# Optimization experiments

Measured on AMD Instinct MI355X. Metric: run time of the kernel, lower is better.

## Reference

```python
import jax, jax.numpy as jnp
import numpy as np

H = 64   # LSTM hidden size
NL = 8   # LSTM layers
B, T = 2048, 64


def setup_inputs() -> dict:
    key = jax.random.key(0)
    ks = jax.random.split(key, 18)
    r = lambda i, shape, s=0.1: jax.random.normal(ks[i], shape, dtype=jnp.float32) * s
    return {
        "x": r(0, (B, T, 2), 1.0),
        "w1": r(1, (16, 2)), "b1": r(2, (16,)),
        "w2": r(3, (16, 16)), "b2": r(4, (16,)),
        "w_ih0": r(5, (4 * H, 16)), "w_hh0": r(6, (4 * H, H)),
        "b_ih0": r(7, (4 * H,)), "b_hh0": r(8, (4 * H,)),
        "w_ih": r(9, (NL - 1, 4 * H, H)), "w_hh": r(10, (NL - 1, 4 * H, H)),
        "b_ih": r(11, (NL - 1, 4 * H)), "b_hh": r(12, (NL - 1, 4 * H)),
        "wo1": r(13, (32, H)), "bo1": r(14, (32,)),
        "wo2": r(15, (4, 32)), "bo2": r(16, (4,)),
    }


def _lstm_layer(x, w_ih, w_hh, b):
    # x: [B, T, I]; torch gate order: i, f, g, o
    bsz = x.shape[0]
    xg = jnp.einsum('bti,gi->btg', x, w_ih) + b  # [B, T, 4H] precomputed input gates

    def step(carry, xg_t):
        h, c = carry
        gates = xg_t + h @ w_hh.T
        i, f, g, o = jnp.split(gates, 4, axis=-1)
        i = jax.nn.sigmoid(i); f = jax.nn.sigmoid(f)
        g = jnp.tanh(g); o = jax.nn.sigmoid(o)
        c = f * c + i * g
        h = o * jnp.tanh(c)
        return (h, c), h

    h0 = jnp.zeros((bsz, H), x.dtype)
    _, hs = jax.lax.scan(step, (h0, h0), jnp.swapaxes(xg, 0, 1))  # [T, B, H]
    return jnp.swapaxes(hs, 0, 1)


def reference(x, w1, b1, w2, b2, w_ih0, w_hh0, b_ih0, b_hh0,
              w_ih, w_hh, b_ih, b_hh, wo1, bo1, wo2, bo2):
    # action-input MLP: 2 -> 16 -> relu -> 16
    h = jax.nn.relu(x @ w1.T + b1) @ w2.T + b2
    # 8-layer LSTM, hidden 64
    h = _lstm_layer(h, w_ih0, w_hh0, b_ih0 + b_hh0)
    for l in range(NL - 1):
        h = _lstm_layer(h, w_ih[l], w_hh[l], b_ih[l] + b_hh[l])
    # output MLP: 64 -> 32 -> relu -> 4
    return jax.nn.relu(h @ wo1.T + bo1) @ wo2.T + bo2
```

## Files before the change

kernel.cpp:

```cpp
#include <hip/hip_runtime.h>


#define BATCH 2048
#define TT 64
#define HH 64
#define LDP 136

typedef short bf16x8 __attribute__((ext_vector_type(8)));
typedef float f32x4 __attribute__((ext_vector_type(4)));

__device__ __forceinline__ float sigmoid_fast(float x) {
    return __builtin_amdgcn_rcpf(1.f + __expf(-x));
}
__device__ __forceinline__ float tanh_fast(float x) {
    float e = __expf(-2.f * x);
    e = fminf(e, 1e30f);
    return (1.f - e) * __builtin_amdgcn_rcpf(1.f + e);
}
__device__ __forceinline__ void split2(float x, unsigned short& hi, unsigned short& lo) {
    const unsigned u = __float_as_uint(x);
    hi = (unsigned short)(u >> 16);
    const float r = x - __uint_as_float(u & 0xFFFF0000u);
    lo = (unsigned short)(__float_as_uint(r) >> 16);
}
__device__ __forceinline__ void wg_wait(int* c, int v) {
    while (__hip_atomic_load(c, __ATOMIC_ACQUIRE, __HIP_MEMORY_SCOPE_WORKGROUP) < v) {}
}
__device__ __forceinline__ void wg_bump(int* c, int lane) {
    if (lane == 0)
        __hip_atomic_fetch_add(c, 1, __ATOMIC_RELEASE, __HIP_MEMORY_SCOPE_WORKGROUP);
}

__global__ __launch_bounds__(256)
void mlp_in_kernel(const float* __restrict__ x,
                   const float* __restrict__ w1, const float* __restrict__ b1,
                   const float* __restrict__ w2, const float* __restrict__ b2,
                   float* __restrict__ out) {
    const int gid = blockIdx.x * 256 + threadIdx.x;
    const float x0 = x[gid * 2 + 0];
    const float x1 = x[gid * 2 + 1];
    float hid[16];
#pragma unroll
    for (int j = 0; j < 16; ++j) {
        float v = fmaf(x1, w1[j * 2 + 1], fmaf(x0, w1[j * 2 + 0], b1[j]));
        hid[j] = fmaxf(0.f, v);
    }
    float o[16];
#pragma unroll
    for (int oo = 0; oo < 16; ++oo) {
        float acc = b2[oo];
#pragma unroll
        for (int j = 0; j < 16; ++j) acc = fmaf(hid[j], w2[oo * 16 + j], acc);
        o[oo] = acc;
    }
    float4* op = (float4*)(out + gid * 16);
#pragma unroll
    for (int q = 0; q < 4; ++q) {
        float4 v;
        v.x = o[q * 4 + 0]; v.y = o[q * 4 + 1]; v.z = o[q * 4 + 2]; v.w = o[q * 4 + 3];
        op[q] = v;
    }
}

template <int IA, int IPADA>
__global__ __launch_bounds__(512, 2)
void lstm_pair(const float* __restrict__ xmlp,
               unsigned* __restrict__ P,
               float* __restrict__ houtf,
               const int last,
               const float* __restrict__ wihA, const float* __restrict__ whhA,
               const float* __restrict__ biA, const float* __restrict__ bhA,
               const float* __restrict__ wihB, const float* __restrict__ whhB,
               const float* __restrict__ biB, const float* __restrict__ bhB) {
    constexpr int KTA = (IPADA + 64) / 32;
    constexpr int KTX = IPADA / 32;
    constexpr int LDPA = IPADA + 8;
    __shared__ __align__(16) unsigned short pAh[2][16 * LDPA], pAl[2][16 * LDPA];
    __shared__ __align__(16) unsigned short pBh[2][16 * LDP], pBl[2][16 * LDP];
    __shared__ int cA, cB;

    const int tid = threadIdx.x;
    const int wv = tid >> 6, lane = tid & 63, l16 = lane & 15, quad = lane >> 4;
    const int grp = wv >> 2;
    const int wg = wv & 3;
    const int base = blockIdx.x * 8;
    const bool lo32 = (lane < 32);
    const int bpi = (lane & 31) << 2;

    if (tid == 0) { cA = 0; cB = 0; }
    for (int e = tid; e < 2 * 16 * LDPA; e += 512) { (&pAh[0][0])[e] = 0; (&pAl[0][0])[e] = 0; }
    for (int e = tid; e < 2 * 16 * LDP; e += 512)  { (&pBh[0][0])[e] = 0; (&pBl[0][0])[e] = 0; }

    const int I    = grp ? 64 : IA;
    const int IPAD = grp ? 64 : IPADA;
    const int KT   = grp ? 4  : KTA;
    const float* wih = grp ? wihB : wihA;
    const float* whh = grp ? whhB : whhA;
    const float* bi  = grp ? biB  : biA;
    const float* bh  = grp ? bhB  : bhA;

    const int jg = 16 * wg + l16;
    bf16x8 bhi[4][4], blo[4][4];
    float bsum[4];
#pragma unroll
    for (int gt = 0; gt < 4; ++gt) {
        const int n = gt * 64 + jg;
        bsum[gt] = bi[n] + bh[n];
#pragma unroll
        for (int kt = 0; kt < 4; ++kt) {
            bf16x8 vh = {0, 0, 0, 0, 0, 0, 0, 0};
            bf16x8 vl = {0, 0, 0, 0, 0, 0, 0, 0};
            if (kt < KT) {
#pragma unroll
                for (int j = 0; j < 8; ++j) {
                    const int k = kt * 32 + quad * 8 + j;
                    float w = 0.f;
                    if (k < I) w = wih[n * I + k];
                    else if (k >= IPAD) w = whh[n * 64 + (k - IPAD)];
                    unsigned short h_, l_;
                    split2(w, h_, l_);
                    vh[j] = (short)h_;
                    vl[j] = (short)l_;
                }
            }
            bhi[kt][gt] = vh;
            blo[kt][gt] = vl;
        }
    }

    float cs[2] = {0.f, 0.f};
    const int row0 = (quad & 1) * 4 + ((quad >> 1) << 1);

    float2 xr2 = {0.f, 0.f};
    uint2 xru = {0u, 0u};
    int sr = 0, sc = 0;
    bool stg = false;
    if (grp == 0) {
        if (IA == 16) {
            stg = (tid < 128);
            sr = tid >> 3; sc = (tid & 7) * 2;
            if (stg) {
                xr2 = *(const float2*)&xmlp[((size_t)(base + sr) * TT + 0) * 16 + sc];
                unsigned short h0, l0, h1, l1;
                split2(xr2.x, h0, l0); split2(xr2.y, h1, l1);
                *(unsigned*)&pAh[0][sr * LDPA + sc] = ((unsigned)h1 << 16) | h0;
                *(unsigned*)&pAl[0][sr * LDPA + sc] = ((unsigned)l1 << 16) | l0;
                xr2 = *(const float2*)&xmlp[((size_t)(base + sr) * TT + 1) * 16 + sc];
            }
        } else {
            stg = true;
            sr = tid >> 5; sc = (tid & 31) * 2;
            xru = *(const uint2*)&P[((size_t)(base + sr) * TT + 0) * 64 + sc];
            *(unsigned*)&pAh[0][sr * LDPA + sc] = (xru.y & 0xFFFF0000u) | (xru.x >> 16);
            *(unsigned*)&pAl[0][sr * LDPA + sc] = (xru.y << 16) | (xru.x & 0xFFFFu);
            xru = *(const uint2*)&P[((size_t)(base + sr) * TT + 1) * 64 + sc];
        }
    }
    __syncthreads();

    if (grp == 0) {
        for (int t = 0; t < TT; ++t) {
            const int pb = t & 1;
            if (t) {
                wg_wait(&cA, 4 * t);
                if (t >= 2) wg_wait(&cB, 4 * (t - 1));
            }
            if (stg) {
                if (IA == 16) {
                    unsigned short h0, l0, h1, l1;
                    split2(xr2.x, h0, l0); split2(xr2.y, h1, l1);
                    *(unsigned*)&pAh[pb ^ 1][sr * LDPA + sc] = ((unsigned)h1 << 16) | h0;
                    *(unsigned*)&pAl[pb ^ 1][sr * LDPA + sc] = ((unsigned)l1 << 16) | l0;
                    const int tp = (t + 2) & (TT - 1);
                    xr2 = *(const float2*)&xmlp[((size_t)(base + sr) * TT + tp) * 16 + sc];
                } else {
                    *(unsigned*)&pAh[pb ^ 1][sr * LDPA + sc] = (xru.y & 0xFFFF0000u) | (xru.x >> 16);
                    *(unsigned*)&pAl[pb ^ 1][sr * LDPA + sc] = (xru.y << 16) | (xru.x & 0xFFFFu);
                    const int tp = (t + 2) & (TT - 1);
                    xru = *(const uint2*)&P[((size_t)(base + sr) * TT + tp) * 64 + sc];
                }
            }
            f32x4 a0[4], a1[4], a2[4];
#pragma unroll
            for (int gt = 0; gt < 4; ++gt) {
                a0[gt][0] = bsum[gt]; a0[gt][1] = bsum[gt];
                a0[gt][2] = bsum[gt]; a0[gt][3] = bsum[gt];
                a1[gt] = (f32x4){0.f, 0.f, 0.f, 0.f};
                a2[gt] = (f32x4){0.f, 0.f, 0.f, 0.f};
            }
            __builtin_amdgcn_s_setprio(1);
#pragma unroll
            for (int kt = 0; kt < KTA; ++kt) {
                bf16x8 ahi, alo;
                if (kt < KTX) {
                    const int aoff = l16 * LDPA + kt * 32 + quad * 8;
                    ahi = *(const bf16x8*)&pAh[pb][aoff];
                    alo = *(const bf16x8*)&pAl[pb][aoff];
                } else {
                    const int aoff = l16 * LDP + (kt - KTX) * 32 + quad * 8;
                    ahi = *(const bf16x8*)&pBh[pb ^ 1][aoff];
                    alo = *(const bf16x8*)&pBl[pb ^ 1][aoff];
                }
#pragma unroll
                for (int gt = 0; gt < 4; ++gt) {
                    a0[gt] = __builtin_amdgcn_mfma_f32_16x16x32_bf16(ahi, bhi[kt][gt], a0[gt], 0, 0, 0);
                    a1[gt] = __builtin_amdgcn_mfma_f32_16x16x32_bf16(alo, bhi[kt][gt], a1[gt], 0, 0, 0);
                    a2[gt] = __builtin_amdgcn_mfma_f32_16x16x32_bf16(ahi, blo[kt][gt], a2[gt], 0, 0, 0);
                }
            }
            __builtin_amdgcn_s_setprio(0);
            f32x4 s4[4];
#pragma unroll
            for (int gt = 0; gt < 4; ++gt) s4[gt] = (a0[gt] + a1[gt]) + a2[gt];
            float gk[4][2];
#pragma unroll
            for (int gt = 0; gt < 4; ++gt) {
#pragma unroll
                for (int r = 0; r < 2; ++r) {
                    const float up = __uint_as_float(
                        __builtin_amdgcn_ds_bpermute(bpi, __float_as_uint(s4[gt][r + 2])));
                    gk[gt][r] = lo32 ? s4[gt][r] : up;
                }
            }
#pragma unroll
            for (int r = 0; r < 2; ++r) {
                const float iv = sigmoid_fast(gk[0][r]);
                const float fv = sigmoid_fast(gk[1][r]);
                const float gv = tanh_fast(gk[2][r]);
                const float ov = sigmoid_fast(gk[3][r]);
                const float cn = fv * cs[r] + iv * gv;
                cs[r] = cn;
                const float h = ov * tanh_fast(cn);
                const int R = row0 + r;
                unsigned short h_, l_;
                split2(h, h_, l_);
                pBh[pb][R * LDP + jg] = h_;
                pBl[pb][R * LDP + jg] = l_;
            }
            wg_bump(&cA, lane);
        }
    } else {
        for (int t = 0; t < TT; ++t) {
            const int pb = t & 1;
            wg_wait(&cA, 4 * (t + 1));
            if (t) wg_wait(&cB, 4 * t);
            f32x4 a0[4], a1[4], a2[4];
#pragma unroll
            for (int gt = 0; gt < 4; ++gt) {
                a0[gt][0] = bsum[gt]; a0[gt][1] = bsum[gt];
                a0[gt][2] = bsum[gt]; a0[gt][3] = bsum[gt];
                a1[gt] = (f32x4){0.f, 0.f, 0.f, 0.f};
                a2[gt] = (f32x4){0.f, 0.f, 0.f, 0.f};
            }
            __builtin_amdgcn_s_setprio(1);
#pragma unroll
            for (int kt = 0; kt < 4; ++kt) {
                const int aoff = l16 * LDP + kt * 32 + quad * 8;
                const bf16x8 ahi = *(const bf16x8*)&pBh[pb][aoff];
                const bf16x8 alo = *(const bf16x8*)&pBl[pb][aoff];
#pragma unroll
                for (int gt = 0; gt < 4; ++gt) {
                    a0[gt] = __builtin_amdgcn_mfma_f32_16x16x32_bf16(ahi, bhi[kt][gt], a0[gt], 0, 0, 0);
                    a1[gt] = __builtin_amdgcn_mfma_f32_16x16x32_bf16(alo, bhi[kt][gt], a1[gt], 0, 0, 0);
                    a2[gt] = __builtin_amdgcn_mfma_f32_16x16x32_bf16(ahi, blo[kt][gt], a2[gt], 0, 0, 0);
                }
            }
            __builtin_amdgcn_s_setprio(0);
            f32x4 s4[4];
#pragma unroll
            for (int gt = 0; gt < 4; ++gt) s4[gt] = (a0[gt] + a1[gt]) + a2[gt];
            float gk[4][2];
#pragma unroll
            for (int gt = 0; gt < 4; ++gt) {
#pragma unroll
                for (int r = 0; r < 2; ++r) {
                    const float up = __uint_as_float(
                        __builtin_amdgcn_ds_bpermute(bpi, __float_as_uint(s4[gt][r + 2])));
                    gk[gt][r] = lo32 ? s4[gt][r] : up;
                }
            }
#pragma unroll
            for (int r = 0; r < 2; ++r) {
                const float iv = sigmoid_fast(gk[0][r]);
                const float fv = sigmoid_fast(gk[1][r]);
                const float gv = tanh_fast(gk[2][r]);
                const float ov = sigmoid_fast(gk[3][r]);
                const float cn = fv * cs[r] + iv * gv;
                cs[r] = cn;
                const float h = ov * tanh_fast(cn);
                const int R = row0 + r;
                unsigned short h_, l_;
                split2(h, h_, l_);
                pBh[pb ^ 1][R * LDP + 64 + jg] = h_;
                pBl[pb ^ 1][R * LDP + 64 + jg] = l_;
                if (!last) {
                    P[((size_t)(base + R) * TT + t) * 64 + jg] =
                        ((unsigned)h_ << 16) | (unsigned)l_;
                } else {
                    houtf[((size_t)(base + R) * TT + t) * HH + jg] = h;
                }
            }
            wg_bump(&cB, lane);
        }
    }
}

__global__ __launch_bounds__(256)
void mlp_out_kernel(const float* __restrict__ hin,
                    const float* __restrict__ wo1, const float* __restrict__ bo1,
                    const float* __restrict__ wo2, const float* __restrict__ bo2,
                    float* __restrict__ out) {
    __shared__ __align__(16) float wo1_s[32 * 64];
    __shared__ float bo1_s[32];
    __shared__ float wo2_s[4 * 32];
    __shared__ float bo2_s[4];
    const int tid = threadIdx.x;
    for (int e = tid; e < 32 * 64; e += 256) wo1_s[e] = wo1[e];
    if (tid < 32) bo1_s[tid] = bo1[tid];
    if (tid < 128) wo2_s[tid] = wo2[tid];
    if (tid < 4) bo2_s[tid] = bo2[tid];
    __syncthreads();

    const int gid = blockIdx.x * 256 + tid;
    const float4* hv = (const float4*)(hin + gid * 64);
    float4 h[16];
#pragma unroll
    for (int q = 0; q < 16; ++q) h[q] = hv[q];

    float m1[32];
#pragma unroll
    for (int o = 0; o < 32; ++o) {
        float acc = bo1_s[o];
        const float4* wrow = (const float4*)(wo1_s + o * 64);
#pragma unroll
        for (int q = 0; q < 16; ++q) {
            const float4 w = wrow[q];
            acc = fmaf(h[q].x, w.x, acc);
            acc = fmaf(h[q].y, w.y, acc);
            acc = fmaf(h[q].z, w.z, acc);
            acc = fmaf(h[q].w, w.w, acc);
        }
        m1[o] = fmaxf(0.f, acc);
    }
    float r[4];
#pragma unroll
    for (int q = 0; q < 4; ++q) {
        float acc = bo2_s[q];
#pragma unroll
        for (int o = 0; o < 32; ++o) acc = fmaf(m1[o], wo2_s[q * 32 + o], acc);
        r[q] = acc;
    }
    float4 res;
    res.x = r[0]; res.y = r[1]; res.z = r[2]; res.w = r[3];
    ((float4*)out)[gid] = res;
}

extern "C" void kernel_launch(void* const* d_in, const int* in_sizes, int n_in,
                              void* d_out, int out_size, void* d_ws, size_t ws_size,
                              hipStream_t stream) {
    const float* x     = (const float*)d_in[0];
    const float* w1    = (const float*)d_in[1];
    const float* b1    = (const float*)d_in[2];
    const float* w2    = (const float*)d_in[3];
    const float* b2    = (const float*)d_in[4];
    const float* w_ih0 = (const float*)d_in[5];
    const float* w_hh0 = (const float*)d_in[6];
    const float* b_ih0 = (const float*)d_in[7];
    const float* b_hh0 = (const float*)d_in[8];
    const float* w_ih  = (const float*)d_in[9];
    const float* w_hh  = (const float*)d_in[10];
    const float* b_ih  = (const float*)d_in[11];
    const float* b_hh  = (const float*)d_in[12];
    const float* wo1   = (const float*)d_in[13];
    const float* bo1   = (const float*)d_in[14];
    const float* wo2   = (const float*)d_in[15];
    const float* bo2   = (const float*)d_in[16];

    float* buf_mlp = (float*)d_ws;
    unsigned* P = (unsigned*)(buf_mlp + (size_t)BATCH * TT * 16);
    float* bufH = (float*)(P + (size_t)BATCH * TT * 64);

    const int nbt_blocks = (BATCH * TT) / 256;

    mlp_in_kernel<<<nbt_blocks, 256, 0, stream>>>(x, w1, b1, w2, b2, buf_mlp);

    lstm_pair<16, 32><<<BATCH / 8, 512, 0, stream>>>(
        buf_mlp, P, bufH, 0,
        w_ih0, w_hh0, b_ih0, b_hh0,
        w_ih + (size_t)0 * 256 * 64, w_hh + (size_t)0 * 256 * 64, b_ih + 0 * 256, b_hh + 0 * 256);

    for (int p = 1; p < 4; ++p) {
        const int la = 2 * p - 1, lb = 2 * p;
        lstm_pair<64, 64><<<BATCH / 8, 512, 0, stream>>>(
            buf_mlp, P, bufH, (p == 3) ? 1 : 0,
            w_ih + (size_t)la * 256 * 64, w_hh + (size_t)la * 256 * 64,
            b_ih + la * 256, b_hh + la * 256,
            w_ih + (size_t)lb * 256 * 64, w_hh + (size_t)lb * 256 * 64,
            b_ih + lb * 256, b_hh + lb * 256);
    }

    mlp_out_kernel<<<nbt_blocks, 256, 0, stream>>>(bufH, wo1, bo1, wo2, bo2, (float*)d_out);
}
```

Measured before the change: 518.1 us.

## Add early-release counter so layer A waits only for B's reads, not B's step

Adds a new shared counter that group B bumps right after loading its input h tiles from LDS into registers, before its MFMAs. Group A now waits on that counter only just before writing its new hidden state, instead of waiting on B's full step completion at the top of each iteration. This loosens the coupling between the two pipelined layers so A's matmul and activations can overlap B's compute. A-operand loads are also hoisted out of the MFMA loop in both groups, and the layer-0 staging row index is masked with sr&7. The change adds one more spin-wait and more registers per thread, which may increase register pressure under launch_bounds(512,2).

```diff
diff --git a/kernel.cpp b/kernel.cpp
--- a/kernel.cpp
+++ b/kernel.cpp
@@ -77,7 +77,7 @@
     constexpr int LDPA = IPADA + 8;
     __shared__ __align__(16) unsigned short pAh[2][16 * LDPA], pAl[2][16 * LDPA];
     __shared__ __align__(16) unsigned short pBh[2][16 * LDP], pBl[2][16 * LDP];
-    __shared__ int cA, cB;
+    __shared__ int cA, cB, cBm;
 
     const int tid = threadIdx.x;
     const int wv = tid >> 6, lane = tid & 63, l16 = lane & 15, quad = lane >> 4;
@@ -87,7 +87,7 @@
     const bool lo32 = (lane < 32);
     const int bpi = (lane & 31) << 2;
 
-    if (tid == 0) { cA = 0; cB = 0; }
+    if (tid == 0) { cA = 0; cB = 0; cBm = 0; }
     for (int e = tid; e < 2 * 16 * LDPA; e += 512) { (&pAh[0][0])[e] = 0; (&pAl[0][0])[e] = 0; }
     for (int e = tid; e < 2 * 16 * LDP; e += 512)  { (&pBh[0][0])[e] = 0; (&pBl[0][0])[e] = 0; }
 
@@ -133,27 +133,29 @@
 
     float2 xr2 = {0.f, 0.f};
     uint2 xru = {0u, 0u};
-    int sr = 0, sc = 0;
+    int sr = 0, sc = 0, srd = 0;
     bool stg = false;
     if (grp == 0) {
         if (IA == 16) {
             stg = (tid < 128);
             sr = tid >> 3; sc = (tid & 7) * 2;
+            srd = base + (sr & 7);
             if (stg) {
-                xr2 = *(const float2*)&xmlp[((size_t)(base + sr) * TT + 0) * 16 + sc];
+                xr2 = *(const float2*)&xmlp[((size_t)srd * TT + 0) * 16 + sc];
                 unsigned short h0, l0, h1, l1;
                 split2(xr2.x, h0, l0); split2(xr2.y, h1, l1);
                 *(unsigned*)&pAh[0][sr * LDPA + sc] = ((unsigned)h1 << 16) | h0;
                 *(unsigned*)&pAl[0][sr * LDPA + sc] = ((unsigned)l1 << 16) | l0;
-                xr2 = *(const float2*)&xmlp[((size_t)(base + sr) * TT + 1) * 16 + sc];
+                xr2 = *(const float2*)&xmlp[((size_t)srd * TT + 1) * 16 + sc];
             }
         } else {
             stg = true;
             sr = tid >> 5; sc = (tid & 31) * 2;
-            xru = *(const uint2*)&P[((size_t)(base + sr) * TT + 0) * 64 + sc];
+            srd = base + sr;
+            xru = *(const uint2*)&P[((size_t)srd * TT + 0) * 64 + sc];
             *(unsigned*)&pAh[0][sr * LDPA + sc] = (xru.y & 0xFFFF0000u) | (xru.x >> 16);
             *(unsigned*)&pAl[0][sr * LDPA + sc] = (xru.y << 16) | (xru.x & 0xFFFFu);
-            xru = *(const uint2*)&P[((size_t)(base + sr) * TT + 1) * 64 + sc];
+            xru = *(const uint2*)&P[((size_t)srd * TT + 1) * 64 + sc];
         }
     }
     __syncthreads();
@@ -161,10 +163,7 @@
     if (grp == 0) {
         for (int t = 0; t < TT; ++t) {
             const int pb = t & 1;
-            if (t) {
-                wg_wait(&cA, 4 * t);
-                if (t >= 2) wg_wait(&cB, 4 * (t - 1));
-            }
+            if (t) wg_wait(&cA, 4 * t);
             if (stg) {
                 if (IA == 16) {
                     unsigned short h0, l0, h1, l1;
@@ -172,12 +171,25 @@
                     *(unsigned*)&pAh[pb ^ 1][sr * LDPA + sc] = ((unsigned)h1 << 16) | h0;
                     *(unsigned*)&pAl[pb ^ 1][sr * LDPA + sc] = ((unsigned)l1 << 16) | l0;
                     const int tp = (t + 2) & (TT - 1);
-                    xr2 = *(const float2*)&xmlp[((size_t)(base + sr) * TT + tp) * 16 + sc];
+                    xr2 = *(const float2*)&xmlp[((size_t)srd * TT + tp) * 16 + sc];
                 } else {
                     *(unsigned*)&pAh[pb ^ 1][sr * LDPA + sc] = (xru.y & 0xFFFF0000u) | (xru.x >> 16);
                     *(unsigned*)&pAl[pb ^ 1][sr * LDPA + sc] = (xru.y << 16) | (xru.x & 0xFFFFu);
                     const int tp = (t + 2) & (TT - 1);
-                    xru = *(const uint2*)&P[((size_t)(base + sr) * TT + tp) * 64 + sc];
+                    xru = *(const uint2*)&P[((size_t)srd * TT + tp) * 64 + sc];
+                }
+            }
+            bf16x8 ahi[4], alo[4];
+#pragma unroll
+            for (int kt = 0; kt < KTA; ++kt) {
+                if (kt < KTX) {
+                    const int aoff = l16 * LDPA + kt * 32 + quad * 8;
+                    ahi[kt] = *(const bf16x8*)&pAh[pb][aoff];
+                    alo[kt] = *(const bf16x8*)&pAl[pb][aoff];
+                } else {
+                    const int aoff = l16 * LDP + (kt - KTX) * 32 + quad * 8;
+                    ahi[kt] = *(const bf16x8*)&pBh[pb ^ 1][aoff];
+                    alo[kt] = *(const bf16x8*)&pBl[pb ^ 1][aoff];
                 }
             }
             f32x4 a0[4], a1[4], a2[4];
@@ -191,21 +203,11 @@
             __builtin_amdgcn_s_setprio(1);
 #pragma unroll
             for (int kt = 0; kt < KTA; ++kt) {
-                bf16x8 ahi, alo;
-                if (kt < KTX) {
-                    const int aoff = l16 * LDPA + kt * 32 + quad * 8;
-                    ahi = *(const bf16x8*)&pAh[pb][aoff];
-                    alo = *(const bf16x8*)&pAl[pb][aoff];
-                } else {
-                    const int aoff = l16 * LDP + (kt - KTX) * 32 + quad * 8;
-                    ahi = *(const bf16x8*)&pBh[pb ^ 1][aoff];
-                    alo = *(const bf16x8*)&pBl[pb ^ 1][aoff];
-                }
 #pragma unroll
                 for (int gt = 0; gt < 4; ++gt) {
-                    a0[gt] = __builtin_amdgcn_mfma_f32_16x16x32_bf16(ahi, bhi[kt][gt], a0[gt], 0, 0, 0);
-                    a1[gt] = __builtin_amdgcn_mfma_f32_16x16x32_bf16(alo, bhi[kt][gt], a1[gt], 0, 0, 0);
-                    a2[gt] = __builtin_amdgcn_mfma_f32_16x16x32_bf16(ahi, blo[kt][gt], a2[gt], 0, 0, 0);
+                    a0[gt] = __builtin_amdgcn_mfma_f32_16x16x32_bf16(ahi[kt], bhi[kt][gt], a0[gt], 0, 0, 0);
+                    a1[gt] = __builtin_amdgcn_mfma_f32_16x16x32_bf16(alo[kt], bhi[kt][gt], a1[gt], 0, 0, 0);
+                    a2[gt] = __builtin_amdgcn_mfma_f32_16x16x32_bf16(ahi[kt], blo[kt][gt], a2[gt], 0, 0, 0);
                 }
             }
             __builtin_amdgcn_s_setprio(0);
@@ -222,6 +224,7 @@
                     gk[gt][r] = lo32 ? s4[gt][r] : up;
                 }
             }
+            float hv[2];
 #pragma unroll
             for (int r = 0; r < 2; ++r) {
                 const float iv = sigmoid_fast(gk[0][r]);
@@ -230,10 +233,14 @@
                 const float ov = sigmoid_fast(gk[3][r]);
                 const float cn = fv * cs[r] + iv * gv;
                 cs[r] = cn;
-                const float h = ov * tanh_fast(cn);
+                hv[r] = ov * tanh_fast(cn);
+            }
+            if (t >= 2) wg_wait(&cBm, 4 * (t - 1));
+#pragma unroll
+            for (int r = 0; r < 2; ++r) {
                 const int R = row0 + r;
                 unsigned short h_, l_;
-                split2(h, h_, l_);
+                split2(hv[r], h_, l_);
                 pBh[pb][R * LDP + jg] = h_;
                 pBl[pb][R * LDP + jg] = l_;
             }
@@ -242,8 +249,16 @@
     } else {
         for (int t = 0; t < TT; ++t) {
             const int pb = t & 1;
+            if (t) wg_wait(&cB, 4 * t);
             wg_wait(&cA, 4 * (t + 1));
-            if (t) wg_wait(&cB, 4 * t);
+            bf16x8 ahi[4], alo[4];
+#pragma unroll
+            for (int kt = 0; kt < 4; ++kt) {
+                const int aoff = l16 * LDP + kt * 32 + quad * 8;
+                ahi[kt] = *(const bf16x8*)&pBh[pb][aoff];
+                alo[kt] = *(const bf16x8*)&pBl[pb][aoff];
+            }
+            wg_bump(&cBm, lane);
             f32x4 a0[4], a1[4], a2[4];
 #pragma unroll
             for (int gt = 0; gt < 4; ++gt) {
@@ -255,14 +270,11 @@
             __builtin_amdgcn_s_setprio(1);
 #pragma unroll
             for (int kt = 0; kt < 4; ++kt) {
-                const int aoff = l16 * LDP + kt * 32 + quad * 8;
-                const bf16x8 ahi = *(const bf16x8*)&pBh[pb][aoff];
-                const bf16x8 alo = *(const bf16x8*)&pBl[pb][aoff];
 #pragma unroll
                 for (int gt = 0; gt < 4; ++gt) {
-                    a0[gt] = __builtin_amdgcn_mfma_f32_16x16x32_bf16(ahi, bhi[kt][gt], a0[gt], 0, 0, 0);
-                    a1[gt] = __builtin_amdgcn_mfma_f32_16x16x32_bf16(alo, bhi[kt][gt], a1[gt], 0, 0, 0);
-                    a2[gt] = __builtin_amdgcn_mfma_f32_16x16x32_bf16(ahi, blo[kt][gt], a2[gt], 0, 0, 0);
+                    a0[gt] = __builtin_amdgcn_mfma_f32_16x16x32_bf16(ahi[kt], bhi[kt][gt], a0[gt], 0, 0, 0);
+                    a1[gt] = __builtin_amdgcn_mfma_f32_16x16x32_bf16(alo[kt], bhi[kt][gt], a1[gt], 0, 0, 0);
+                    a2[gt] = __builtin_amdgcn_mfma_f32_16x16x32_bf16(ahi[kt], blo[kt][gt], a2[gt], 0, 0, 0);
                 }
             }
             __builtin_amdgcn_s_setprio(0);
```

Result: slower. 535.4 us (+3.3%).
